# Optimization experiments

Hardware: AMD Instinct MI355X
Metric: run time of the kernel (lower is better)

## Reference

```python
import jax, jax.numpy as jnp
import numpy as np

N, NFEAT, NHID, NCLASS, NLAYERS = 8192, 512, 128, 40, 3
NEG = -9e15

def _sparse_adj(key, n, density=0.002):
    u = jax.random.uniform(key, (n, n), dtype=jnp.float32)
    return jnp.where(u < density, u / density, 0.0)

def setup_inputs() -> dict:
    key = jax.random.key(0)
    ks = jax.random.split(key, 12)
    return {
        "x": jax.random.normal(ks[0], (N, NFEAT), dtype=jnp.float32),
        "adj1": _sparse_adj(ks[1], N),
        "adj2": _sparse_adj(ks[2], N),
        "adj_att": _sparse_adj(ks[3], N),
        "fc1_w": jax.random.normal(ks[4], (NLAYERS, NHID, NFEAT), dtype=jnp.float32) * (1.0 / np.sqrt(NFEAT)),
        "fc1_b": jnp.zeros((NLAYERS, NHID), jnp.float32),
        "Q_w": jax.random.normal(ks[5], (NLAYERS - 1, NHID, NHID), dtype=jnp.float32) * (1.0 / np.sqrt(NHID)),
        "Q_b": jnp.zeros((NLAYERS - 1, NHID), jnp.float32),
        "K_w": jax.random.normal(ks[6], (NLAYERS - 1, NHID, NHID), dtype=jnp.float32) * (1.0 / np.sqrt(NHID)),
        "K_b": jnp.zeros((NLAYERS - 1, NHID), jnp.float32),
        "hop_select": jnp.ones((NLAYERS,), jnp.float32),
        "w": jnp.ones((NLAYERS - 1, 2), jnp.float32),
        "clf_w": jax.random.normal(ks[7], (NCLASS, NHID * NLAYERS), dtype=jnp.float32) * (1.0 / np.sqrt(NHID * NLAYERS)),
        "clf_b": jnp.zeros((NCLASS,), jnp.float32),
    }

def _l2_normalize(x, eps=1e-12):
    # F.normalize(x, p=2, dim=1)
    n = jnp.sqrt(jnp.sum(x * x, axis=1, keepdims=True))
    return x / jnp.maximum(n, eps)

def reference(x, adj1, adj2, adj_att, fc1_w, fc1_b, Q_w, Q_b, K_w, K_b,
              hop_select, w, clf_w, clf_b):
    adj_list = [None, adj1, adj2]
    mask = jax.nn.softmax(hop_select)  # hop selection weights, shape [nlayers]
    outs = []
    for i in range(NLAYERS):
        tmp = x @ fc1_w[i].T + fc1_b[i]  # [N, nhid]
        if adj_list[i] is not None:
            adj = adj_list[i]
            W_att = jax.nn.softmax(w[i - 1])  # [2]
            tmp_att = adj_att @ tmp           # [N, nhid]
            # GCN1: linear then propagate with adj_att (act='None')
            Q = adj_att @ (tmp_att @ Q_w[i - 1].T + Q_b[i - 1])
            K = adj_att @ (tmp_att @ K_w[i - 1].T + K_b[i - 1])
            scores = Q @ K.T                  # [N, N]
            scores = jnp.where(adj > 0, scores, NEG)
            attention = jax.nn.softmax(scores, axis=-1) * W_att[0] + adj * W_att[1]
            tmp = attention @ tmp             # [N, nhid]
        tmp = _l2_normalize(tmp)
        outs.append(mask[i] * tmp)
    final = jnp.concatenate(outs, axis=1)     # [N, nhid*nlayers]
    out = jax.nn.relu(final) @ clf_w.T + clf_b  # dropout is identity in eval
    return jax.nn.log_softmax(out, axis=1)
```

## Files before the change

### kernel.cpp

```cpp
#include <hip/hip_runtime.h>
#include <hip/hip_bf16.h>

#define NN     8192
#define NF4    2048
#define NFEAT  512
#define NHID   128
#define NCLASS 40
#define NLAY   3
#define CAPA   128
#define FSZ    ((size_t)NN * NHID)

typedef float f32x4 __attribute__((ext_vector_type(4)));

__global__ void k_setup(const float* __restrict__ hop, const float* __restrict__ w,
                        float* __restrict__ mask, float* __restrict__ watt,
                        float* __restrict__ colsum) {
    int t = threadIdx.x;
    colsum[t] = 0.f;
    if (t == 0) {
        float m = fmaxf(fmaxf(hop[0], hop[1]), hop[2]);
        float e0 = expf(hop[0] - m), e1 = expf(hop[1] - m), e2 = expf(hop[2] - m);
        float s = e0 + e1 + e2;
        mask[0] = e0 / s; mask[1] = e1 / s; mask[2] = e2 / s;
        for (int l = 0; l < 2; ++l) {
            float a = w[2 * l], b = w[2 * l + 1];
            float mm = fmaxf(a, b);
            float ea = expf(a - mm), eb = expf(b - mm);
            float ss = ea + eb;
            watt[2 * l] = ea / ss; watt[2 * l + 1] = eb / ss;
        }
    }
}

__global__ __launch_bounds__(256, 4) void k_gemm_fc1(
    const float* __restrict__ A, const float* __restrict__ B,
    const float* __restrict__ bias, float* __restrict__ tmps, float* __restrict__ colsum)
{
    __shared__ float smem[2176 + 4224];
    float* As = smem;
    float* Bs = smem + 2176;
    const int tid = threadIdx.x, tx = tid & 15, ty = tid >> 4;
    const int bm = blockIdx.x * 64;
    const int layer = blockIdx.y;
    const int bn = layer * 128;
    float acc[4][8] = {};

    for (int kt = 0; kt < NFEAT; kt += 32) {
        #pragma unroll
        for (int it = 0; it < 2; ++it) {
            int L = tid + it * 256;
            int r = L >> 3, c4 = (L & 7) * 4;
            f32x4 va = *reinterpret_cast<const f32x4*>(&A[(size_t)(bm + r) * NFEAT + kt + c4]);
            As[(c4 + 0) * 68 + r] = va[0];
            As[(c4 + 1) * 68 + r] = va[1];
            As[(c4 + 2) * 68 + r] = va[2];
            As[(c4 + 3) * 68 + r] = va[3];
        }
        #pragma unroll
        for (int it = 0; it < 4; ++it) {
            int L = tid + it * 256;
            int r = L >> 3, c4 = (L & 7) * 4;
            f32x4 vb = *reinterpret_cast<const f32x4*>(&B[(size_t)(bn + r) * NFEAT + kt + c4]);
            Bs[(c4 + 0) * 132 + r] = vb[0];
            Bs[(c4 + 1) * 132 + r] = vb[1];
            Bs[(c4 + 2) * 132 + r] = vb[2];
            Bs[(c4 + 3) * 132 + r] = vb[3];
        }
        __syncthreads();
        #pragma unroll
        for (int kk = 0; kk < 32; ++kk) {
            f32x4 ra  = *reinterpret_cast<const f32x4*>(&As[kk * 68 + ty * 4]);
            f32x4 rb0 = *reinterpret_cast<const f32x4*>(&Bs[kk * 132 + tx * 4]);
            f32x4 rb1 = *reinterpret_cast<const f32x4*>(&Bs[kk * 132 + tx * 4 + 64]);
            #pragma unroll
            for (int i = 0; i < 4; ++i) {
                #pragma unroll
                for (int j = 0; j < 4; ++j) {
                    acc[i][j]     = fmaf(ra[i], rb0[j], acc[i][j]);
                    acc[i][j + 4] = fmaf(ra[i], rb1[j], acc[i][j + 4]);
                }
            }
        }
        __syncthreads();
    }
    const float* bofs = bias + bn;
    #pragma unroll
    for (int i = 0; i < 4; ++i) {
        int m = bm + ty * 4 + i;
        #pragma unroll
        for (int j = 0; j < 8; ++j) {
            int lc = (j < 4) ? (tx * 4 + j) : (64 + tx * 4 + (j - 4));
            tmps[(size_t)layer * FSZ + (size_t)m * NHID + lc] = acc[i][j] + bofs[lc];
        }
    }
    if (layer >= 1) {
        #pragma unroll
        for (int j = 0; j < 8; ++j) {
            int lc = (j < 4) ? (tx * 4 + j) : (64 + tx * 4 + (j - 4));
            float s = 4.f * bofs[lc];
            #pragma unroll
            for (int i = 0; i < 4; ++i) s += acc[i][j];
            smem[ty * 128 + lc] = s;
        }
        __syncthreads();
        if (tid < 128) {
            float s = 0.f;
            #pragma unroll
            for (int g = 0; g < 16; ++g) s += smem[g * 128 + tid];
            atomicAdd(&colsum[(layer - 1) * NHID + tid], s);
        }
    }
}

__global__ __launch_bounds__(256) void k_extract3(
    const float* __restrict__ adjA, const float* __restrict__ adj1, const float* __restrict__ adj2,
    int* __restrict__ cnts, int* __restrict__ colsArr, float* __restrict__ valsArr,
    float* __restrict__ rowsumA)
{
    const int row = blockIdx.x, mat = blockIdx.y, tid = threadIdx.x;
    const float* adj = (mat == 0) ? adjA : (mat == 1 ? adj1 : adj2);
    __shared__ int s_lcnt;
    __shared__ float s_lsum;
    if (tid == 0) { s_lcnt = 0; s_lsum = 0.f; }
    __syncthreads();
    const f32x4* arow = reinterpret_cast<const f32x4*>(adj + (size_t)row * NN);
    int* rc = colsArr + (size_t)(mat * NN + row) * CAPA;
    float* rv = valsArr + (size_t)(mat * NN + row) * CAPA;
    float ls = 0.f;
    for (int c4 = tid; c4 < NF4; c4 += 256) {
        f32x4 v = __builtin_nontemporal_load(&arow[c4]);
        #pragma unroll
        for (int k = 0; k < 4; ++k) {
            if (v[k] > 0.f) {
                int p = atomicAdd(&s_lcnt, 1);
                if (p < CAPA) { rc[p] = c4 * 4 + k; rv[p] = v[k]; }
                ls += v[k];
            }
        }
    }
    if (mat == 0 && ls != 0.f) atomicAdd(&s_lsum, ls);
    __syncthreads();
    if (tid == 0) {
        cnts[mat * NN + row] = s_lcnt < CAPA ? s_lcnt : CAPA;
        if (mat == 0) rowsumA[row] = s_lsum;
    }
}

__global__ __launch_bounds__(128) void k_sp_norm(
    const int* __restrict__ cnts, const int* __restrict__ colsArr, const float* __restrict__ valsArr,
    const float* __restrict__ tmps, const float* __restrict__ mask,
    float* __restrict__ tmp_att, float* __restrict__ outsb)
{
    int row = blockIdx.x, role = blockIdx.y, t = threadIdx.x;
    __shared__ int sc[CAPA];
    __shared__ float sv[CAPA];
    __shared__ float wsn[2];
    if (role == 2) {
        float v = tmps[(size_t)row * NHID + t];
        float s = v * v;
        #pragma unroll
        for (int m = 32; m; m >>= 1) s += __shfl_xor(s, m);
        if ((t & 63) == 0) wsn[t >> 6] = s;
        __syncthreads();
        float d = fmaxf(sqrtf(wsn[0] + wsn[1]), 1e-12f);
        outsb[(size_t)row * (NHID * NLAY) + t] = mask[0] * v / d;
    } else {
        const float* X = tmps + (size_t)(role + 1) * FSZ;
        float* Y = tmp_att + (size_t)role * FSZ;
        int n = cnts[row];
        for (int p = t; p < n; p += 128) { sc[p] = colsArr[(size_t)row * CAPA + p]; sv[p] = valsArr[(size_t)row * CAPA + p]; }
        __syncthreads();
        float a0 = 0.f, a1 = 0.f;
        int p = 0;
        for (; p + 2 <= n; p += 2) {
            a0 = fmaf(sv[p],     X[(size_t)sc[p]     * NHID + t], a0);
            a1 = fmaf(sv[p + 1], X[(size_t)sc[p + 1] * NHID + t], a1);
        }
        if (p < n) a0 = fmaf(sv[p], X[(size_t)sc[p] * NHID + t], a0);
        Y[(size_t)row * NHID + t] = a0 + a1;
    }
}

__global__ __launch_bounds__(128) void k_spmm2(
    const int* __restrict__ cnts, const int* __restrict__ colsArr, const float* __restrict__ valsArr,
    const float* __restrict__ X, float* __restrict__ Y)
{
    int row = blockIdx.x, L = blockIdx.y, t = threadIdx.x;
    const float* Xl = X + (size_t)L * FSZ;
    float* Yl = Y + (size_t)L * FSZ;
    __shared__ int sc[CAPA];
    __shared__ float sv[CAPA];
    int n = cnts[row];
    for (int p = t; p < n; p += 128) { sc[p] = colsArr[(size_t)row * CAPA + p]; sv[p] = valsArr[(size_t)row * CAPA + p]; }
    __syncthreads();
    float a0 = 0.f, a1 = 0.f;
    int p = 0;
    for (; p + 2 <= n; p += 2) {
        a0 = fmaf(sv[p],     Xl[(size_t)sc[p]     * NHID + t], a0);
        a1 = fmaf(sv[p + 1], Xl[(size_t)sc[p + 1] * NHID + t], a1);
    }
    if (p < n) a0 = fmaf(sv[p], Xl[(size_t)sc[p] * NHID + t], a0);
    Yl[(size_t)row * NHID + t] = a0 + a1;
}

__global__ __launch_bounds__(256) void k_gemm_qkm(
    const float* __restrict__ T2, const float* __restrict__ Qw, const float* __restrict__ Kw,
    const float* __restrict__ Qb, const float* __restrict__ Kb,
    const float* __restrict__ rowsumA, float* __restrict__ QKm)
{
    __shared__ float As[64][68];
    __shared__ float Bs[64][68];
    const int tid = threadIdx.x, tx = tid & 15, ty = tid >> 4;
    const int bm = blockIdx.x * 64, bn = blockIdx.y * 64, Lz = blockIdx.z;
    const float* A = T2 + (size_t)Lz * FSZ;
    const float* Bp; const float* bp; int bc;
    if (bn < 128) { Bp = Qw + (size_t)Lz * NHID * NHID; bp = Qb + (size_t)Lz * NHID; bc = bn; }
    else          { Bp = Kw + (size_t)Lz * NHID * NHID; bp = Kb + (size_t)Lz * NHID; bc = bn - 128; }
    float* C = QKm + (size_t)Lz * NN * 256;
    float acc[4][4] = {};

    for (int kt = 0; kt < NHID; kt += 64) {
        #pragma unroll
        for (int it = 0; it < 4; ++it) {
            int L = tid + it * 256;
            int r = L >> 4, c4 = (L & 15) * 4;
            f32x4 va = *reinterpret_cast<const f32x4*>(&A[(size_t)(bm + r) * NHID + kt + c4]);
            As[c4 + 0][r] = va[0]; As[c4 + 1][r] = va[1]; As[c4 + 2][r] = va[2]; As[c4 + 3][r] = va[3];
            f32x4 vb = *reinterpret_cast<const f32x4*>(&Bp[(size_t)(bc + r) * NHID + kt + c4]);
            Bs[c4 + 0][r] = vb[0]; Bs[c4 + 1][r] = vb[1]; Bs[c4 + 2][r] = vb[2]; Bs[c4 + 3][r] = vb[3];
        }
        __syncthreads();
        #pragma unroll
        for (int kk = 0; kk < 64; ++kk) {
            f32x4 ra4 = *reinterpret_cast<const f32x4*>(&As[kk][ty * 4]);
            f32x4 rb4 = *reinterpret_cast<const f32x4*>(&Bs[kk][tx * 4]);
            #pragma unroll
            for (int i = 0; i < 4; ++i)
                #pragma unroll
                for (int j = 0; j < 4; ++j)
                    acc[i][j] = fmaf(ra4[i], rb4[j], acc[i][j]);
        }
        __syncthreads();
    }
    #pragma unroll
    for (int i = 0; i < 4; ++i) {
        int m = bm + ty * 4 + i;
        float rs = rowsumA[m];
        #pragma unroll
        for (int j = 0; j < 4; ++j) {
            int n = bn + tx * 4 + j;
            C[(size_t)m * 256 + n] = acc[i][j] + rs * bp[bc + tx * 4 + j];
        }
    }
}

__global__ __launch_bounds__(256) void k_attn(
    const int* __restrict__ cnts, const int* __restrict__ colsArr, const float* __restrict__ valsArr,
    const float* __restrict__ QKm, const float* __restrict__ tmps,
    const float* __restrict__ colsum, const float* __restrict__ watt,
    const float* __restrict__ mask, float* __restrict__ outsb)
{
    int row = blockIdx.x, L = blockIdx.y, t = threadIdx.x;
    const float* QK = QKm + (size_t)L * NN * 256;
    const float* T = tmps + (size_t)(L + 1) * FSZ;
    const int* rc = colsArr + (size_t)((1 + L) * NN + row) * CAPA;
    const float* rv = valsArr + (size_t)((1 + L) * NN + row) * CAPA;
    __shared__ int cols[CAPA];
    __shared__ float avals[CAPA];
    __shared__ float svals[CAPA];
    __shared__ __align__(16) float qrow[NHID];
    __shared__ float psum[2][NHID];
    __shared__ float ws[4];

    int n = cnts[(1 + L) * NN + row];
    for (int p = t; p < n; p += 256) { cols[p] = rc[p]; avals[p] = rv[p]; }
    if (t < 32) *reinterpret_cast<f32x4*>(&qrow[t * 4]) =
        *reinterpret_cast<const f32x4*>(QK + (size_t)row * 256 + t * 4);
    __syncthreads();

    float W0 = watt[L * 2], W1 = watt[L * 2 + 1];
    float acc = 0.f;

    if (n > 0) {
        int g = t >> 5, sl = t & 31;
        f32x4 qv = *reinterpret_cast<const f32x4*>(&qrow[sl * 4]);
        for (int p = g; p < n; p += 8) {
            f32x4 kv = *reinterpret_cast<const f32x4*>(QK + (size_t)cols[p] * 256 + 128 + sl * 4);
            float s = qv[0] * kv[0] + qv[1] * kv[1] + qv[2] * kv[2] + qv[3] * kv[3];
            #pragma unroll
            for (int m = 16; m; m >>= 1) s += __shfl_xor(s, m);
            if (sl == 0) svals[p] = s;
        }
        __syncthreads();
        if (t < 64) {
            float mx = -3.0e38f;
            for (int p = t; p < n; p += 64) mx = fmaxf(mx, svals[p]);
            #pragma unroll
            for (int m = 32; m; m >>= 1) mx = fmaxf(mx, __shfl_xor(mx, m));
            float ss = 0.f;
            for (int p = t; p < n; p += 64) ss += expf(svals[p] - mx);
            #pragma unroll
            for (int m = 32; m; m >>= 1) ss += __shfl_xor(ss, m);
            float inv = 1.0f / ss;
            for (int p = t; p < n; p += 64) avals[p] = expf(svals[p] - mx) * inv * W0 + avals[p] * W1;
        }
        __syncthreads();
        int half = t >> 7, tt = t & 127;
        float pacc = 0.f;
        for (int p = half; p < n; p += 2) pacc = fmaf(avals[p], T[(size_t)cols[p] * NHID + tt], pacc);
        psum[half][tt] = pacc;
        __syncthreads();
        if (t < 128) acc = psum[0][t] + psum[1][t];
    } else {
        if (t < 128) acc = W0 * (1.0f / (float)NN) * colsum[L * NHID + t];
    }

    float s2 = acc * acc;
    #pragma unroll
    for (int m = 32; m; m >>= 1) s2 += __shfl_xor(s2, m);
    if ((t & 63) == 0) ws[t >> 6] = s2;
    __syncthreads();
    if (t < 128) {
        float d = fmaxf(sqrtf(ws[0] + ws[1]), 1e-12f);
        outsb[(size_t)row * (NHID * NLAY) + (size_t)(L + 1) * NHID + t] = mask[L + 1] * acc / d;
    }
}

__global__ __launch_bounds__(64) void k_clf(
    const float* __restrict__ outs, const float* __restrict__ Wc,
    const float* __restrict__ bc, float* __restrict__ out)
{
    __shared__ float fin[NHID * NLAY];
    __shared__ float logits[NCLASS];
    int t = threadIdx.x;
    for (int rr = 0; rr < 2; ++rr) {
        int row = blockIdx.x * 2 + rr;
        for (int k = t; k < NHID * NLAY; k += 64) fin[k] = fmaxf(outs[(size_t)row * (NHID * NLAY) + k], 0.f);
        __syncthreads();
        if (t < NCLASS) {
            float acc = bc[t];
            #pragma unroll 4
            for (int k = 0; k < NHID * NLAY; ++k) acc = fmaf(fin[k], Wc[(size_t)t * (NHID * NLAY) + k], acc);
            logits[t] = acc;
        }
        __syncthreads();
        float x = (t < NCLASS) ? logits[t] : -3.0e38f;
        float mx = x;
        #pragma unroll
        for (int m = 32; m; m >>= 1) mx = fmaxf(mx, __shfl_xor(mx, m));
        float e = (t < NCLASS) ? expf(x - mx) : 0.f;
        float ssum = e;
        #pragma unroll
        for (int m = 32; m; m >>= 1) ssum += __shfl_xor(ssum, m);
        if (t < NCLASS) out[(size_t)row * NCLASS + t] = x - mx - logf(ssum);
        __syncthreads();
    }
}

extern "C" void kernel_launch(void* const* d_in, const int* in_sizes, int n_in,
                              void* d_out, int out_size, void* d_ws, size_t ws_size,
                              hipStream_t stream) {
    const float* x       = (const float*)d_in[0];
    const float* adj1    = (const float*)d_in[1];
    const float* adj2    = (const float*)d_in[2];
    const float* adj_att = (const float*)d_in[3];
    const float* fc1_w   = (const float*)d_in[4];
    const float* fc1_b   = (const float*)d_in[5];
    const float* Q_w     = (const float*)d_in[6];
    const float* Q_b     = (const float*)d_in[7];
    const float* K_w     = (const float*)d_in[8];
    const float* K_b     = (const float*)d_in[9];
    const float* hop     = (const float*)d_in[10];
    const float* w       = (const float*)d_in[11];
    const float* clf_w   = (const float*)d_in[12];
    const float* clf_b   = (const float*)d_in[13];

    float* W = (float*)d_ws;
    float* f_mask   = W;
    float* f_watt   = W + 4;
    float* f_colsum = W + 8;
    float* rowsumA  = W + 264;
    float* tmps     = W + 264 + NN;
    float* outsb    = tmps + 3 * FSZ;
    float* tmp_att  = outsb + 3 * FSZ;
    float* T2b      = tmp_att + 2 * FSZ;
    float* QKm      = T2b + 2 * FSZ;
    float* csr_vals = QKm + 4 * FSZ;
    int*   csr_cols = (int*)(csr_vals + 3 * FSZ);
    int*   csr_cnt  = csr_cols + 3 * FSZ;

    size_t need = (size_t)((char*)(csr_cnt + 3 * NN) - (char*)d_ws);
    if (ws_size < need) return;

    k_setup<<<1, 256, 0, stream>>>(hop, w, f_mask, f_watt, f_colsum);

    k_gemm_fc1<<<dim3(NN / 64, 3), 256, 0, stream>>>(x, fc1_w, fc1_b, tmps, f_colsum);

    k_extract3<<<dim3(NN, 3), 256, 0, stream>>>(
        adj_att, adj1, adj2, csr_cnt, csr_cols, csr_vals, rowsumA);

    k_sp_norm<<<dim3(NN, 3), 128, 0, stream>>>(
        csr_cnt, csr_cols, csr_vals, tmps, f_mask, tmp_att, outsb);

    k_spmm2<<<dim3(NN, 2), 128, 0, stream>>>(csr_cnt, csr_cols, csr_vals, tmp_att, T2b);

    k_gemm_qkm<<<dim3(NN / 64, 4, 2), 256, 0, stream>>>(T2b, Q_w, K_w, Q_b, K_b, rowsumA, QKm);

    k_attn<<<dim3(NN, 2), 256, 0, stream>>>(
        csr_cnt, csr_cols, csr_vals, QKm, tmps, f_colsum, f_watt, f_mask, outsb);

    k_clf<<<NN / 2, 64, 0, stream>>>(outsb, clf_w, clf_b, (float*)d_out);
}
```

Measured before the change: 380.8 us.

## Fuse fc1 GEMM with adjacency scan, and fuse second SpMM into QK GEMM

Merges the fc1 GEMM and the dense adjacency CSR extraction into one launch, so the GEMM blocks overlap the bandwidth-bound scan. Fuses the second sparse propagation (adj_att @ tmp_att) directly into the Q/K projection GEMM, keeping the intermediate in shared memory. This removes the T2 buffer round trip and one launch. The sp_norm gather loop is unrolled to four accumulators. Risks: the fused t2qkm kernel has only 256 blocks and runs a serial per-thread gather, so occupancy is lower. It also uses 64KB of shared memory per block.

```diff
diff --git a/kernel.cpp b/kernel.cpp
--- a/kernel.cpp
+++ b/kernel.cpp
@@ -32,117 +32,117 @@
     }
 }
 
-__global__ __launch_bounds__(256, 4) void k_gemm_fc1(
-    const float* __restrict__ A, const float* __restrict__ B,
-    const float* __restrict__ bias, float* __restrict__ tmps, float* __restrict__ colsum)
+__global__ __launch_bounds__(256, 4) void k_scan_fc1(
+    const float* __restrict__ x, const float* __restrict__ fc1w, const float* __restrict__ fc1b,
+    const float* __restrict__ adjA, const float* __restrict__ adj1, const float* __restrict__ adj2,
+    float* __restrict__ tmps, float* __restrict__ colsum, float* __restrict__ rowsumA,
+    int* __restrict__ cnts, int* __restrict__ colsArr, float* __restrict__ valsArr)
 {
-    __shared__ float smem[2176 + 4224];
-    float* As = smem;
-    float* Bs = smem + 2176;
-    const int tid = threadIdx.x, tx = tid & 15, ty = tid >> 4;
-    const int bm = blockIdx.x * 64;
-    const int layer = blockIdx.y;
-    const int bn = layer * 128;
-    float acc[4][8] = {};
-
-    for (int kt = 0; kt < NFEAT; kt += 32) {
-        #pragma unroll
-        for (int it = 0; it < 2; ++it) {
-            int L = tid + it * 256;
-            int r = L >> 3, c4 = (L & 7) * 4;
-            f32x4 va = *reinterpret_cast<const f32x4*>(&A[(size_t)(bm + r) * NFEAT + kt + c4]);
-            As[(c4 + 0) * 68 + r] = va[0];
-            As[(c4 + 1) * 68 + r] = va[1];
-            As[(c4 + 2) * 68 + r] = va[2];
-            As[(c4 + 3) * 68 + r] = va[3];
-        }
-        #pragma unroll
-        for (int it = 0; it < 4; ++it) {
-            int L = tid + it * 256;
-            int r = L >> 3, c4 = (L & 7) * 4;
-            f32x4 vb = *reinterpret_cast<const f32x4*>(&B[(size_t)(bn + r) * NFEAT + kt + c4]);
-            Bs[(c4 + 0) * 132 + r] = vb[0];
-            Bs[(c4 + 1) * 132 + r] = vb[1];
-            Bs[(c4 + 2) * 132 + r] = vb[2];
-            Bs[(c4 + 3) * 132 + r] = vb[3];
-        }
-        __syncthreads();
-        #pragma unroll
-        for (int kk = 0; kk < 32; ++kk) {
-            f32x4 ra  = *reinterpret_cast<const f32x4*>(&As[kk * 68 + ty * 4]);
-            f32x4 rb0 = *reinterpret_cast<const f32x4*>(&Bs[kk * 132 + tx * 4]);
-            f32x4 rb1 = *reinterpret_cast<const f32x4*>(&Bs[kk * 132 + tx * 4 + 64]);
-            #pragma unroll
-            for (int i = 0; i < 4; ++i) {
-                #pragma unroll
-                for (int j = 0; j < 4; ++j) {
-                    acc[i][j]     = fmaf(ra[i], rb0[j], acc[i][j]);
-                    acc[i][j + 4] = fmaf(ra[i], rb1[j], acc[i][j + 4]);
-                }
-            }
-        }
-        __syncthreads();
-    }
-    const float* bofs = bias + bn;
-    #pragma unroll
-    for (int i = 0; i < 4; ++i) {
-        int m = bm + ty * 4 + i;
-        #pragma unroll
-        for (int j = 0; j < 8; ++j) {
-            int lc = (j < 4) ? (tx * 4 + j) : (64 + tx * 4 + (j - 4));
-            tmps[(size_t)layer * FSZ + (size_t)m * NHID + lc] = acc[i][j] + bofs[lc];
-        }
-    }
-    if (layer >= 1) {
-        #pragma unroll
-        for (int j = 0; j < 8; ++j) {
-            int lc = (j < 4) ? (tx * 4 + j) : (64 + tx * 4 + (j - 4));
-            float s = 4.f * bofs[lc];
-            #pragma unroll
-            for (int i = 0; i < 4; ++i) s += acc[i][j];
-            smem[ty * 128 + lc] = s;
-        }
-        __syncthreads();
-        if (tid < 128) {
-            float s = 0.f;
-            #pragma unroll
-            for (int g = 0; g < 16; ++g) s += smem[g * 128 + tid];
-            atomicAdd(&colsum[(layer - 1) * NHID + tid], s);
-        }
-    }
-}
-
-__global__ __launch_bounds__(256) void k_extract3(
-    const float* __restrict__ adjA, const float* __restrict__ adj1, const float* __restrict__ adj2,
-    int* __restrict__ cnts, int* __restrict__ colsArr, float* __restrict__ valsArr,
-    float* __restrict__ rowsumA)
-{
-    const int row = blockIdx.x, mat = blockIdx.y, tid = threadIdx.x;
-    const float* adj = (mat == 0) ? adjA : (mat == 1 ? adj1 : adj2);
+    __shared__ float smem[6400];
     __shared__ int s_lcnt;
     __shared__ float s_lsum;
-    if (tid == 0) { s_lcnt = 0; s_lsum = 0.f; }
-    __syncthreads();
-    const f32x4* arow = reinterpret_cast<const f32x4*>(adj + (size_t)row * NN);
-    int* rc = colsArr + (size_t)(mat * NN + row) * CAPA;
-    float* rv = valsArr + (size_t)(mat * NN + row) * CAPA;
-    float ls = 0.f;
-    for (int c4 = tid; c4 < NF4; c4 += 256) {
-        f32x4 v = __builtin_nontemporal_load(&arow[c4]);
-        #pragma unroll
-        for (int k = 0; k < 4; ++k) {
-            if (v[k] > 0.f) {
-                int p = atomicAdd(&s_lcnt, 1);
-                if (p < CAPA) { rc[p] = c4 * 4 + k; rv[p] = v[k]; }
-                ls += v[k];
-            }
-        }
-    }
-    if (mat == 0 && ls != 0.f) atomicAdd(&s_lsum, ls);
-    __syncthreads();
-    if (tid == 0) {
-        cnts[mat * NN + row] = s_lcnt < CAPA ? s_lcnt : CAPA;
-        if (mat == 0) rowsumA[row] = s_lsum;
+    const int bx = blockIdx.x, plane = blockIdx.y, tid = threadIdx.x;
+
+    if (bx < 128) {
+        float* As = smem;
+        float* Bs = smem + 2176;
+        const int tx = tid & 15, ty = tid >> 4;
+        const int bm = bx * 64;
+        const int layer = plane;
+        const int bn = layer * 128;
+        float acc[4][8] = {};
+
+        for (int kt = 0; kt < NFEAT; kt += 32) {
+            #pragma unroll
+            for (int it = 0; it < 2; ++it) {
+                int L = tid + it * 256;
+                int r = L >> 3, c4 = (L & 7) * 4;
+                f32x4 va = *reinterpret_cast<const f32x4*>(&x[(size_t)(bm + r) * NFEAT + kt + c4]);
+                As[(c4 + 0) * 68 + r] = va[0];
+                As[(c4 + 1) * 68 + r] = va[1];
+                As[(c4 + 2) * 68 + r] = va[2];
+                As[(c4 + 3) * 68 + r] = va[3];
+            }
+            #pragma unroll
+            for (int it = 0; it < 4; ++it) {
+                int L = tid + it * 256;
+                int r = L >> 3, c4 = (L & 7) * 4;
+                f32x4 vb = *reinterpret_cast<const f32x4*>(&fc1w[(size_t)(bn + r) * NFEAT + kt + c4]);
+                Bs[(c4 + 0) * 132 + r] = vb[0];
+                Bs[(c4 + 1) * 132 + r] = vb[1];
+                Bs[(c4 + 2) * 132 + r] = vb[2];
+                Bs[(c4 + 3) * 132 + r] = vb[3];
+            }
+            __syncthreads();
+            #pragma unroll
+            for (int kk = 0; kk < 32; ++kk) {
+                f32x4 ra  = *reinterpret_cast<const f32x4*>(&As[kk * 68 + ty * 4]);
+                f32x4 rb0 = *reinterpret_cast<const f32x4*>(&Bs[kk * 132 + tx * 4]);
+                f32x4 rb1 = *reinterpret_cast<const f32x4*>(&Bs[kk * 132 + tx * 4 + 64]);
+                #pragma unroll
+                for (int i = 0; i < 4; ++i) {
+                    #pragma unroll
+                    for (int j = 0; j < 4; ++j) {
+                        acc[i][j]     = fmaf(ra[i], rb0[j], acc[i][j]);
+                        acc[i][j + 4] = fmaf(ra[i], rb1[j], acc[i][j + 4]);
+                    }
+                }
+            }
+            __syncthreads();
+        }
+        const float* bofs = fc1b + bn;
+        #pragma unroll
+        for (int i = 0; i < 4; ++i) {
+            int m = bm + ty * 4 + i;
+            #pragma unroll
+            for (int j = 0; j < 8; ++j) {
+                int lc = (j < 4) ? (tx * 4 + j) : (64 + tx * 4 + (j - 4));
+                tmps[(size_t)layer * FSZ + (size_t)m * NHID + lc] = acc[i][j] + bofs[lc];
+            }
+        }
+        if (layer >= 1) {
+            #pragma unroll
+            for (int j = 0; j < 8; ++j) {
+                int lc = (j < 4) ? (tx * 4 + j) : (64 + tx * 4 + (j - 4));
+                float s = 4.f * bofs[lc];
+                #pragma unroll
+                for (int i = 0; i < 4; ++i) s += acc[i][j];
+                smem[ty * 128 + lc] = s;
+            }
+            __syncthreads();
+            if (tid < 128) {
+                float s = 0.f;
+                #pragma unroll
+                for (int g = 0; g < 16; ++g) s += smem[g * 128 + tid];
+                atomicAdd(&colsum[(layer - 1) * NHID + tid], s);
+            }
+        }
+    } else {
+        const int row = bx - 128, mat = plane;
+        const float* adj = (mat == 0) ? adjA : (mat == 1 ? adj1 : adj2);
+        if (tid == 0) { s_lcnt = 0; s_lsum = 0.f; }
+        __syncthreads();
+        const f32x4* arow = reinterpret_cast<const f32x4*>(adj + (size_t)row * NN);
+        int* rc = colsArr + (size_t)(mat * NN + row) * CAPA;
+        float* rv = valsArr + (size_t)(mat * NN + row) * CAPA;
+        float ls = 0.f;
+        for (int c4 = tid; c4 < NF4; c4 += 256) {
+            f32x4 v = __builtin_nontemporal_load(&arow[c4]);
+            #pragma unroll
+            for (int k = 0; k < 4; ++k) {
+                if (v[k] > 0.f) {
+                    int p = atomicAdd(&s_lcnt, 1);
+                    if (p < CAPA) { rc[p] = c4 * 4 + k; rv[p] = v[k]; }
+                    ls += v[k];
+                }
+            }
+        }
+        if (mat == 0 && ls != 0.f) atomicAdd(&s_lsum, ls);
+        __syncthreads();
+        if (tid == 0) {
+            cnts[mat * NN + row] = s_lcnt < CAPA ? s_lcnt : CAPA;
+            if (mat == 0) rowsumA[row] = s_lsum;
+        }
     }
 }
 
@@ -170,87 +170,101 @@
         int n = cnts[row];
         for (int p = t; p < n; p += 128) { sc[p] = colsArr[(size_t)row * CAPA + p]; sv[p] = valsArr[(size_t)row * CAPA + p]; }
         __syncthreads();
-        float a0 = 0.f, a1 = 0.f;
+        float a0 = 0.f, a1 = 0.f, a2 = 0.f, a3 = 0.f;
         int p = 0;
-        for (; p + 2 <= n; p += 2) {
+        for (; p + 4 <= n; p += 4) {
             a0 = fmaf(sv[p],     X[(size_t)sc[p]     * NHID + t], a0);
             a1 = fmaf(sv[p + 1], X[(size_t)sc[p + 1] * NHID + t], a1);
-        }
-        if (p < n) a0 = fmaf(sv[p], X[(size_t)sc[p] * NHID + t], a0);
-        Y[(size_t)row * NHID + t] = a0 + a1;
-    }
-}
-
-__global__ __launch_bounds__(128) void k_spmm2(
+            a2 = fmaf(sv[p + 2], X[(size_t)sc[p + 2] * NHID + t], a2);
+            a3 = fmaf(sv[p + 3], X[(size_t)sc[p + 3] * NHID + t], a3);
+        }
+        for (; p < n; ++p) a0 = fmaf(sv[p], X[(size_t)sc[p] * NHID + t], a0);
+        Y[(size_t)row * NHID + t] = (a0 + a1) + (a2 + a3);
+    }
+}
+
+__global__ __launch_bounds__(256, 2) void k_t2qkm(
     const int* __restrict__ cnts, const int* __restrict__ colsArr, const float* __restrict__ valsArr,
-    const float* __restrict__ X, float* __restrict__ Y)
-{
-    int row = blockIdx.x, L = blockIdx.y, t = threadIdx.x;
-    const float* Xl = X + (size_t)L * FSZ;
-    float* Yl = Y + (size_t)L * FSZ;
-    __shared__ int sc[CAPA];
-    __shared__ float sv[CAPA];
-    int n = cnts[row];
-    for (int p = t; p < n; p += 128) { sc[p] = colsArr[(size_t)row * CAPA + p]; sv[p] = valsArr[(size_t)row * CAPA + p]; }
-    __syncthreads();
-    float a0 = 0.f, a1 = 0.f;
-    int p = 0;
-    for (; p + 2 <= n; p += 2) {
-        a0 = fmaf(sv[p],     Xl[(size_t)sc[p]     * NHID + t], a0);
-        a1 = fmaf(sv[p + 1], Xl[(size_t)sc[p + 1] * NHID + t], a1);
-    }
-    if (p < n) a0 = fmaf(sv[p], Xl[(size_t)sc[p] * NHID + t], a0);
-    Yl[(size_t)row * NHID + t] = a0 + a1;
-}
-
-__global__ __launch_bounds__(256) void k_gemm_qkm(
-    const float* __restrict__ T2, const float* __restrict__ Qw, const float* __restrict__ Kw,
+    const float* __restrict__ tmp_att, const float* __restrict__ Qw, const float* __restrict__ Kw,
     const float* __restrict__ Qb, const float* __restrict__ Kb,
     const float* __restrict__ rowsumA, float* __restrict__ QKm)
 {
-    __shared__ float As[64][68];
-    __shared__ float Bs[64][68];
-    const int tid = threadIdx.x, tx = tid & 15, ty = tid >> 4;
-    const int bm = blockIdx.x * 64, bn = blockIdx.y * 64, Lz = blockIdx.z;
-    const float* A = T2 + (size_t)Lz * FSZ;
-    const float* Bp; const float* bp; int bc;
-    if (bn < 128) { Bp = Qw + (size_t)Lz * NHID * NHID; bp = Qb + (size_t)Lz * NHID; bc = bn; }
-    else          { Bp = Kw + (size_t)Lz * NHID * NHID; bp = Kb + (size_t)Lz * NHID; bc = bn - 128; }
+    __shared__ float AsT[128 * 64];
+    __shared__ float Bs[128 * 64];
+    const int tid = threadIdx.x;
+    const int bm = blockIdx.x * 64, Lz = blockIdx.y;
+    const float* X = tmp_att + (size_t)Lz * FSZ;
+
+    {
+        const int lrow = tid >> 2, coff = (tid & 3) * 32;
+        const int row = bm + lrow;
+        f32x4 acc[8] = {};
+        const int n = cnts[row];
+        const int* rc = colsArr + (size_t)row * CAPA;
+        const float* rv = valsArr + (size_t)row * CAPA;
+        for (int p = 0; p < n; ++p) {
+            int c = rc[p];
+            float v = rv[p];
+            const f32x4* src = reinterpret_cast<const f32x4*>(X + (size_t)c * NHID + coff);
+            #pragma unroll
+            for (int j = 0; j < 8; ++j) {
+                f32x4 s = src[j];
+                acc[j][0] = fmaf(v, s[0], acc[j][0]);
+                acc[j][1] = fmaf(v, s[1], acc[j][1]);
+                acc[j][2] = fmaf(v, s[2], acc[j][2]);
+                acc[j][3] = fmaf(v, s[3], acc[j][3]);
+            }
+        }
+        #pragma unroll
+        for (int j = 0; j < 8; ++j)
+            #pragma unroll
+            for (int q = 0; q < 4; ++q)
+                AsT[(coff + j * 4 + q) * 64 + lrow] = acc[j][q];
+    }
+    __syncthreads();
+
+    const int tx = tid & 15, ty = tid >> 4;
+    float rs[4];
+    #pragma unroll
+    for (int i = 0; i < 4; ++i) rs[i] = rowsumA[bm + ty * 4 + i];
     float* C = QKm + (size_t)Lz * NN * 256;
-    float acc[4][4] = {};
-
-    for (int kt = 0; kt < NHID; kt += 64) {
-        #pragma unroll
-        for (int it = 0; it < 4; ++it) {
-            int L = tid + it * 256;
-            int r = L >> 4, c4 = (L & 15) * 4;
-            f32x4 va = *reinterpret_cast<const f32x4*>(&A[(size_t)(bm + r) * NHID + kt + c4]);
-            As[c4 + 0][r] = va[0]; As[c4 + 1][r] = va[1]; As[c4 + 2][r] = va[2]; As[c4 + 3][r] = va[3];
-            f32x4 vb = *reinterpret_cast<const f32x4*>(&Bp[(size_t)(bc + r) * NHID + kt + c4]);
-            Bs[c4 + 0][r] = vb[0]; Bs[c4 + 1][r] = vb[1]; Bs[c4 + 2][r] = vb[2]; Bs[c4 + 3][r] = vb[3];
-        }
-        __syncthreads();
-        #pragma unroll
-        for (int kk = 0; kk < 64; ++kk) {
-            f32x4 ra4 = *reinterpret_cast<const f32x4*>(&As[kk][ty * 4]);
-            f32x4 rb4 = *reinterpret_cast<const f32x4*>(&Bs[kk][tx * 4]);
+
+    for (int ch = 0; ch < 4; ++ch) {
+        const int bn = ch * 64;
+        const float* Bp; const float* bp; int bc;
+        if (bn < 128) { Bp = Qw + (size_t)Lz * NHID * NHID; bp = Qb + (size_t)Lz * NHID; bc = bn; }
+        else          { Bp = Kw + (size_t)Lz * NHID * NHID; bp = Kb + (size_t)Lz * NHID; bc = bn - 128; }
+        {
+            int r = tid >> 2, c0 = (tid & 3) * 32;
+            #pragma unroll
+            for (int j = 0; j < 8; ++j) {
+                f32x4 v = *reinterpret_cast<const f32x4*>(&Bp[(size_t)(bc + r) * NHID + c0 + j * 4]);
+                #pragma unroll
+                for (int q = 0; q < 4; ++q) Bs[(c0 + j * 4 + q) * 64 + r] = v[q];
+            }
+        }
+        __syncthreads();
+        float acc[4][4] = {};
+        #pragma unroll 8
+        for (int kk = 0; kk < 128; ++kk) {
+            f32x4 ra = *reinterpret_cast<const f32x4*>(&AsT[kk * 64 + ty * 4]);
+            f32x4 rb = *reinterpret_cast<const f32x4*>(&Bs[kk * 64 + tx * 4]);
             #pragma unroll
             for (int i = 0; i < 4; ++i)
                 #pragma unroll
                 for (int j = 0; j < 4; ++j)
-                    acc[i][j] = fmaf(ra4[i], rb4[j], acc[i][j]);
-        }
-        __syncthreads();
-    }
-    #pragma unroll
-    for (int i = 0; i < 4; ++i) {
-        int m = bm + ty * 4 + i;
-        float rs = rowsumA[m];
-        #pragma unroll
-        for (int j = 0; j < 4; ++j) {
-            int n = bn + tx * 4 + j;
-            C[(size_t)m * 256 + n] = acc[i][j] + rs * bp[bc + tx * 4 + j];
-        }
+                    acc[i][j] = fmaf(ra[i], rb[j], acc[i][j]);
+        }
+        #pragma unroll
+        for (int i = 0; i < 4; ++i) {
+            int m = bm + ty * 4 + i;
+            #pragma unroll
+            for (int j = 0; j < 4; ++j) {
+                int nc = bn + tx * 4 + j;
+                C[(size_t)m * 256 + nc] = acc[i][j] + rs[i] * bp[bc + tx * 4 + j];
+            }
+        }
+        __syncthreads();
     }
 }
 
@@ -383,8 +397,7 @@
     float* tmps     = W + 264 + NN;
     float* outsb    = tmps + 3 * FSZ;
     float* tmp_att  = outsb + 3 * FSZ;
-    float* T2b      = tmp_att + 2 * FSZ;
-    float* QKm      = T2b + 2 * FSZ;
+    float* QKm      = tmp_att + 2 * FSZ;
     float* csr_vals = QKm + 4 * FSZ;
     int*   csr_cols = (int*)(csr_vals + 3 * FSZ);
     int*   csr_cnt  = csr_cols + 3 * FSZ;
@@ -394,17 +407,15 @@
 
     k_setup<<<1, 256, 0, stream>>>(hop, w, f_mask, f_watt, f_colsum);
 
-    k_gemm_fc1<<<dim3(NN / 64, 3), 256, 0, stream>>>(x, fc1_w, fc1_b, tmps, f_colsum);
-
-    k_extract3<<<dim3(NN, 3), 256, 0, stream>>>(
-        adj_att, adj1, adj2, csr_cnt, csr_cols, csr_vals, rowsumA);
+    k_scan_fc1<<<dim3(128 + NN, 3), 256, 0, stream>>>(
+        x, fc1_w, fc1_b, adj_att, adj1, adj2,
+        tmps, f_colsum, rowsumA, csr_cnt, csr_cols, csr_vals);
 
     k_sp_norm<<<dim3(NN, 3), 128, 0, stream>>>(
         csr_cnt, csr_cols, csr_vals, tmps, f_mask, tmp_att, outsb);
 
-    k_spmm2<<<dim3(NN, 2), 128, 0, stream>>>(csr_cnt, csr_cols, csr_vals, tmp_att, T2b);
-
-    k_gemm_qkm<<<dim3(NN / 64, 4, 2), 256, 0, stream>>>(T2b, Q_w, K_w, Q_b, K_b, rowsumA, QKm);
+    k_t2qkm<<<dim3(NN / 64, 2), 256, 0, stream>>>(
+        csr_cnt, csr_cols, csr_vals, tmp_att, Q_w, K_w, Q_b, K_b, rowsumA, QKm);
 
     k_attn<<<dim3(NN, 2), 256, 0, stream>>>(
         csr_cnt, csr_cols, csr_vals, QKm, tmps, f_colsum, f_watt, f_mask, outsb);
```

Measured after the change: 373.3 us. About the same (-1.9%).
